# Kernel optimization log

Hardware: AMD Instinct MI355X
Metric: run time of the kernel (lower is better)

Reference implementation:

```python
import jax, jax.numpy as jnp
import numpy as np

B, T, D, H = 128, 512, 1024, 1024


def setup_inputs() -> dict:
    key = jax.random.key(0)
    ks = jax.random.split(key, 9)
    s = 1.0 / np.sqrt(D + H)
    return {
        "inputs": jax.random.normal(ks[0], (B, T, D), dtype=jnp.float32),
        "Wf": jax.random.normal(ks[1], (D + H, H), dtype=jnp.float32) * s,
        "bf": jax.random.normal(ks[2], (H,), dtype=jnp.float32) * s,
        "Wi": jax.random.normal(ks[3], (D + H, H), dtype=jnp.float32) * s,
        "bi": jax.random.normal(ks[4], (H,), dtype=jnp.float32) * s,
        "Wo": jax.random.normal(ks[5], (D + H, H), dtype=jnp.float32) * s,
        "bo": jax.random.normal(ks[6], (H,), dtype=jnp.float32) * s,
        "Wc": jax.random.normal(ks[7], (D + H, H), dtype=jnp.float32) * s,
        "bc": jax.random.normal(ks[8], (H,), dtype=jnp.float32) * s,
    }


def reference(inputs, Wf, bf, Wi, bi, Wo, bo, Wc, bc):
    # inputs: [B, T, D]; gates computed from concat(x_t, h_t) @ W + b.
    # Fuse the 4 gate Linears into one GEMM (same math, single contraction).
    batch = inputs.shape[0]
    hid = Wf.shape[1]
    W = jnp.concatenate([Wf, Wi, Wo, Wc], axis=1)          # [D+H, 4H]
    b = jnp.concatenate([bf, bi, bo, bc])                   # [4H]

    def step(carry, x_t):
        h, c = carry
        z = jnp.concatenate([x_t, h], axis=1) @ W + b        # [B, 4H]
        f, i, o, g = jnp.split(z, 4, axis=1)
        f = jax.nn.sigmoid(f)
        i = jax.nn.sigmoid(i)
        o = jax.nn.sigmoid(o)
        g = jnp.tanh(g)
        c = f * c + i * g
        h = o * jnp.tanh(c)
        return (h, c), h

    h0 = jnp.zeros((batch, hid), dtype=inputs.dtype)
    c0 = jnp.zeros((batch, hid), dtype=inputs.dtype)
    _, hs = jax.lax.scan(step, (h0, c0), jnp.swapaxes(inputs, 0, 1))  # hs: [T, B, H]
    # Original prepends each new hidden state -> outputs are in REVERSE time order.
    return jnp.flip(jnp.swapaxes(hs, 0, 1), axis=1)          # [B, T, H]
```

## Files before the change

### kernel.cpp

```cpp
#include <hip/hip_runtime.h>
#include <hip/hip_bf16.h>

#define Bb 128
#define Tt 512
#define Dd 1024
#define Hh 1024
#define KD 2048
#define CCH 32
#define NCHUNK (Tt / CCH)
#define NBLK 256

typedef __attribute__((ext_vector_type(4))) float f32x4;
typedef __attribute__((ext_vector_type(8))) short s16x8;
typedef __attribute__((address_space(1))) const void gcvoid;
typedef __attribute__((address_space(3))) void lvoid;

__device__ __forceinline__ unsigned short f2bf(float f) {
    union { float f; unsigned u; } v;
    v.f = f;
    unsigned r = v.u + 0x7fffu + ((v.u >> 16) & 1u);
    return (unsigned short)(r >> 16);
}

__device__ __forceinline__ s16x8 cvt8(const float* src) {
    f32x4 a = *reinterpret_cast<const f32x4*>(src);
    f32x4 b = *reinterpret_cast<const f32x4*>(src + 4);
    s16x8 v;
    v[0] = (short)f2bf(a[0]); v[1] = (short)f2bf(a[1]);
    v[2] = (short)f2bf(a[2]); v[3] = (short)f2bf(a[3]);
    v[4] = (short)f2bf(b[0]); v[5] = (short)f2bf(b[1]);
    v[6] = (short)f2bf(b[2]); v[7] = (short)f2bf(b[3]);
    return v;
}

__device__ __forceinline__ float sigf(float x)      { return 1.f / (1.f + __expf(-x)); }
__device__ __forceinline__ float tanhfast(float x)  { return 1.f - 2.f / (1.f + __expf(2.f * x)); }

__device__ __forceinline__ void cstore2(unsigned short* p, unsigned v) {
    asm volatile("global_store_short %0, %1, off sc1" :: "v"(p), "v"(v) : "memory");
}

__device__ __forceinline__ void gbar(unsigned* cntA, unsigned* cntB,
                                     unsigned* flag, int t, int bid) {
    asm volatile("s_waitcnt vmcnt(0)" ::: "memory");
    __syncthreads();
    if (threadIdx.x == 0) {
        unsigned* ca = cntA + ((size_t)t * 8 + (bid & 7)) * 32;
        unsigned o = __hip_atomic_fetch_add(ca, 1u, __ATOMIC_RELAXED, __HIP_MEMORY_SCOPE_AGENT);
        if (o == 31u) {
            unsigned* cb = cntB + (size_t)t * 32;
            unsigned o2 = __hip_atomic_fetch_add(cb, 1u, __ATOMIC_RELAXED, __HIP_MEMORY_SCOPE_AGENT);
            if (o2 == 7u)
                __hip_atomic_store(flag + t, 1u, __ATOMIC_RELAXED, __HIP_MEMORY_SCOPE_AGENT);
        }
        while (__hip_atomic_load(flag + t, __ATOMIC_RELAXED, __HIP_MEMORY_SCOPE_AGENT) == 0u)
            __builtin_amdgcn_s_sleep(1);
    }
    __syncthreads();
}

__global__ __launch_bounds__(256) void zx_gemm(
    const float* __restrict__ X, const unsigned short* __restrict__ Wr,
    const float* __restrict__ bre, float* __restrict__ Zxc, int t0)
{
    __shared__ __align__(16) unsigned short ALds[2][128 * 64];
    __shared__ __align__(16) unsigned short BLds[2][128 * 64];

    const int tid = threadIdx.x, lane = tid & 63, wv = tid >> 6;
    const int wr = wv >> 1, wc = wv & 1;
    const int m0 = (blockIdx.x >> 5) * 128, n0 = (blockIdx.x & 31) * 128;

    f32x4 acc[4][4];
#pragma unroll
    for (int i = 0; i < 4; ++i)
#pragma unroll
        for (int jn = 0; jn < 4; ++jn) acc[i][jn] = 0.f;

    auto stage = [&](int buf, int ki) {
        const int k0 = ki * 64;
#pragma unroll
        for (int i = 0; i < 4; ++i) {
            int slot = i * 256 + tid;
            int r = slot >> 3, cp = slot & 7;
            int c = cp ^ (r & 7);
            int m = m0 + r, b = m >> 5, tc = m & 31;
            const float* src = X + ((size_t)b * Tt + t0 + tc) * Dd + k0 + c * 8;
            *reinterpret_cast<s16x8*>(&ALds[buf][slot * 8]) = cvt8(src);
        }
#pragma unroll
        for (int i = 0; i < 4; ++i) {
            int slot = i * 256 + tid;
            int r = slot >> 3, cp = slot & 7;
            int c = cp ^ (r & 7);
            const unsigned short* src = Wr + (size_t)(n0 + r) * KD + k0 + c * 8;
            __builtin_amdgcn_global_load_lds((gcvoid*)src,
                (lvoid*)&BLds[buf][(i * 256 + wv * 64) * 8], 16, 0, 0);
        }
    };

    auto compute = [&](int buf) {
#pragma unroll
        for (int ks = 0; ks < 2; ++ks) {
            int ck = ks * 4 + (lane >> 4);
            s16x8 af[4], bf8[4];
#pragma unroll
            for (int m = 0; m < 4; ++m) {
                int ra = wr * 64 + m * 16 + (lane & 15);
                af[m] = *reinterpret_cast<const s16x8*>(&ALds[buf][ra * 64 + (ck ^ (ra & 7)) * 8]);
            }
#pragma unroll
            for (int n = 0; n < 4; ++n) {
                int rb = wc * 64 + n * 16 + (lane & 15);
                bf8[n] = *reinterpret_cast<const s16x8*>(&BLds[buf][rb * 64 + (ck ^ (rb & 7)) * 8]);
            }
#pragma unroll
            for (int m = 0; m < 4; ++m)
#pragma unroll
                for (int n = 0; n < 4; ++n)
                    acc[m][n] = __builtin_amdgcn_mfma_f32_16x16x32_bf16(af[m], bf8[n], acc[m][n], 0, 0, 0);
        }
    };

    stage(0, 0);
#pragma unroll 1
    for (int ki = 0; ki < 16; ++ki) {
        __syncthreads();
        if (ki + 1 < 16) stage((ki + 1) & 1, ki + 1);
        compute(ki & 1);
    }

#pragma unroll
    for (int ni = 0; ni < 4; ++ni) {
        int gcol = n0 + wc * 64 + ni * 16 + (lane & 15);
        float bias = bre[gcol];
        int gg = gcol >> 5, nn = gcol & 31;
        int zcol = gg * 32 + (nn & 7) * 4 + (nn >> 3);
#pragma unroll
        for (int mi = 0; mi < 4; ++mi) {
            int rbase = m0 + wr * 64 + mi * 16 + (lane >> 4) * 4;
#pragma unroll
            for (int r = 0; r < 4; ++r)
                Zxc[(size_t)(rbase + r) * 4096 + zcol] = acc[mi][ni][r] + bias;
        }
    }
}

__global__ __launch_bounds__(256) void lstm_chunk(
    const unsigned short* __restrict__ Wr,
    const float* __restrict__ Zxc,
    unsigned short* __restrict__ hring,
    float* __restrict__ cbuf,
    float* __restrict__ out,
    unsigned* __restrict__ cntA,
    unsigned* __restrict__ cntB,
    unsigned* __restrict__ flag,
    int t0)
{
    __shared__ __align__(16) unsigned short Bl[32 * 1024];

    const int tid = threadIdx.x, lane = tid & 63, w = tid >> 6;
    const int bid = blockIdx.x;
    const int g = bid >> 1, mh = bid & 1;

#pragma unroll
    for (int i = 0; i < 16; ++i) {
        int q = (w * 16 + i) * 64 + lane;
        int n = q >> 7, cp = q & 127;
        int cs = (cp & ~7) | ((cp ^ n) & 7);
        const unsigned short* src = Wr + (size_t)(g * 32 + n) * KD + Dd + cs * 8;
        __builtin_amdgcn_global_load_lds((gcvoid*)src,
            (lvoid*)&Bl[(w * 16 + i) * 512], 16, 0, 0);
    }
    asm volatile("s_waitcnt vmcnt(0)" ::: "memory");
    __syncthreads();

    const int nlo = lane & 15;
    const int r0 = mh * 64 + w * 16 + nlo;
    const unsigned short* b0p = &Bl[nlo * 1024];
    const int jj = lane & 7, j = g * 8 + jj;
    const bool hi = (lane & 8) != 0;
    const int rowb = mh * 64 + w * 16 + (lane >> 4) * 4;

    f32x4 creg;
#pragma unroll
    for (int r = 0; r < 4; ++r)
        creg[r] = cbuf[(size_t)(rowb + r) * Hh + j];

    f32x4 zx[4];
#pragma unroll
    for (int r = 0; r < 4; ++r)
        zx[r] = *reinterpret_cast<const f32x4*>(
            Zxc + ((size_t)(rowb + r) * CCH + 0) * 4096 + j * 4);

#pragma unroll 1
    for (int tt = 0; tt < CCH; ++tt) {
        const int t = t0 + tt;
        const unsigned short* hin = hring + (size_t)(t & (CCH - 1)) * (Bb * Hh);
        unsigned short* houtp = hring + (size_t)((t + 1) & (CCH - 1)) * (Bb * Hh);
        const unsigned short* arow = hin + (size_t)r0 * Hh + (lane >> 4) * 8;

        s16x8 af[32];
#pragma unroll
        for (int ki = 0; ki < 32; ++ki)
            af[ki] = *reinterpret_cast<const s16x8*>(arow + ki * 32);

        f32x4 acc0 = 0.f, acc1 = 0.f;
#pragma unroll
        for (int ki = 0; ki < 32; ++ki) {
            int ck = ki * 4 + (lane >> 4);
            int p = (ck & ~7) | ((ck ^ nlo) & 7);
            s16x8 b0 = *reinterpret_cast<const s16x8*>(b0p + p * 8);
            s16x8 b1 = *reinterpret_cast<const s16x8*>(b0p + 16 * 1024 + p * 8);
            acc0 = __builtin_amdgcn_mfma_f32_16x16x32_bf16(af[ki], b0, acc0, 0, 0, 0);
            acc1 = __builtin_amdgcn_mfma_f32_16x16x32_bf16(af[ki], b1, acc1, 0, 0, 0);
        }

        f32x4 y0, y1;
#pragma unroll
        for (int r = 0; r < 4; ++r) {
            y0[r] = __shfl_xor(acc0[r], 8, 64);
            y1[r] = __shfl_xor(acc1[r], 8, 64);
        }

        f32x4 zxn[4];
        if (tt + 1 < CCH) {
#pragma unroll
            for (int r = 0; r < 4; ++r)
                zxn[r] = *reinterpret_cast<const f32x4*>(
                    Zxc + ((size_t)(rowb + r) * CCH + (tt + 1)) * 4096 + j * 4);
        }

#pragma unroll
        for (int r = 0; r < 4; ++r) {
            float vf = hi ? y0[r] : acc0[r];
            float vi = hi ? acc0[r] : y0[r];
            float vo = hi ? y1[r] : acc1[r];
            float vg = hi ? acc1[r] : y1[r];
            float zf = vf + zx[r][0], zi = vi + zx[r][1];
            float zo = vo + zx[r][2], zc = vg + zx[r][3];
            float fg = sigf(zf), ig = sigf(zi), og = sigf(zo), gv = tanhfast(zc);
            float cnew = fg * creg[r] + ig * gv;
            creg[r] = cnew;
            float hn = og * tanhfast(cnew);
            if (!hi) {
                int row = rowb + r;
                cstore2(houtp + (size_t)row * Hh + j, (unsigned)f2bf(hn));
                out[((size_t)row * Tt + (Tt - 1 - t)) * Hh + j] = hn;
            }
        }
#pragma unroll
        for (int r = 0; r < 4; ++r) zx[r] = zxn[r];

        if (tt + 1 < CCH) gbar(cntA, cntB, flag, t, bid);
    }

    if (!hi) {
#pragma unroll
        for (int r = 0; r < 4; ++r)
            cbuf[(size_t)(rowb + r) * Hh + j] = creg[r];
    }
}

__global__ __launch_bounds__(256) void conv_w(
    const float* __restrict__ Wf, const float* __restrict__ Wi,
    const float* __restrict__ Wo, const float* __restrict__ Wc,
    unsigned short* __restrict__ Wr)
{
    __shared__ float sm[64 * 65];
    const int tid = threadIdx.x;
    const int bid = blockIdx.x;
    const int gate = bid & 3;
    const int rest = bid >> 2;
    const int k0 = (rest & 31) * 64;
    const int c0 = (rest >> 5) * 64;
    const float* Wg = (gate == 0) ? Wf : (gate == 1) ? Wi : (gate == 2) ? Wo : Wc;

#pragma unroll
    for (int it = 0; it < 16; ++it) {
        int kl = it * 4 + (tid >> 6), cl = tid & 63;
        sm[kl * 65 + cl] = Wg[(size_t)(k0 + kl) * Hh + c0 + cl];
    }
    __syncthreads();
#pragma unroll
    for (int it = 0; it < 16; ++it) {
        int nl = it * 4 + (tid >> 6), kl = tid & 63;
        int col = c0 + nl;
        int n = (col >> 3) * 32 + gate * 8 + (col & 7);
        Wr[(size_t)n * KD + k0 + kl] = f2bf(sm[kl * 65 + nl]);
    }
}

#define NBAR_U32 (512 * 8 * 32 + 512 * 32 + 512)

__global__ void init_all(unsigned short* __restrict__ hring, float* __restrict__ cbuf,
                         unsigned* __restrict__ bars, float* __restrict__ bre,
                         const float* __restrict__ bF, const float* __restrict__ bI,
                         const float* __restrict__ bO, const float* __restrict__ bC) {
    int i = blockIdx.x * 256 + threadIdx.x;
    if (i < 2 * Bb * Hh) hring[i] = 0;
    if (i < Bb * Hh) cbuf[i] = 0.f;
    if (i < NBAR_U32) bars[i] = 0u;
    if (i < 4096) {
        int gate = (i >> 3) & 3, g = i >> 5, jjv = i & 7;
        int col = g * 8 + jjv;
        const float* bg = (gate == 0) ? bF : (gate == 1) ? bI : (gate == 2) ? bO : bC;
        bre[i] = bg[col];
    }
}

__global__ __launch_bounds__(256) void lstm_step(
    const float* __restrict__ X, const unsigned short* __restrict__ Wr,
    const float* __restrict__ bre,
    const unsigned short* __restrict__ hin, unsigned short* __restrict__ hout,
    float* __restrict__ cbuf, float* __restrict__ out, int t)
{
    __shared__ __align__(16) unsigned short Alds[2][64 * 64];
    __shared__ __align__(16) unsigned short Blds[2][32 * 64];
    __shared__ float zlds[64 * 33];

    const int tid = threadIdx.x, lane = tid & 63, w = tid >> 6;
    const int g = blockIdx.x >> 1, mh = blockIdx.x & 1;

    f32x4 acc[2];
    acc[0] = 0.f; acc[1] = 0.f;

    auto stageA = [&](int buf, int ki) {
        const int k0 = ki * 64;
#pragma unroll
        for (int i = 0; i < 2; ++i) {
            int slot = tid + 256 * i;
            int r = slot >> 3, cp = slot & 7;
            int c = cp ^ (r & 7);
            int k = k0 + c * 8;
            s16x8 v;
            if (k < Dd) {
                v = cvt8(X + ((size_t)(mh * 64 + r) * Tt + t) * Dd + k);
            } else {
                v = *reinterpret_cast<const s16x8*>(hin + (size_t)(mh * 64 + r) * Hh + (k - Dd));
            }
            *reinterpret_cast<s16x8*>(&Alds[buf][slot * 8]) = v;
        }
    };
    auto stageB = [&](int buf, int ki) {
        int n = tid >> 3, cp = tid & 7;
        int c = cp ^ (n & 7);
        const unsigned short* src = Wr + (size_t)(g * 32 + n) * KD + ki * 64 + c * 8;
        *reinterpret_cast<s16x8*>(&Blds[buf][tid * 8]) = *reinterpret_cast<const s16x8*>(src);
    };
    auto compute = [&](int buf) {
#pragma unroll
        for (int ks = 0; ks < 2; ++ks) {
            int ra = w * 16 + (lane & 15);
            int cha = (ks * 4 + (lane >> 4)) ^ (ra & 7);
            s16x8 af = *reinterpret_cast<const s16x8*>(&Alds[buf][ra * 64 + cha * 8]);
#pragma unroll
            for (int nt = 0; nt < 2; ++nt) {
                int n = nt * 16 + (lane & 15);
                int chb = (ks * 4 + (lane >> 4)) ^ (n & 7);
                s16x8 bf8 = *reinterpret_cast<const s16x8*>(&Blds[buf][n * 64 + chb * 8]);
                acc[nt] = __builtin_amdgcn_mfma_f32_16x16x32_bf16(af, bf8, acc[nt], 0, 0, 0);
            }
        }
    };

    stageA(0, 0); stageB(0, 0);
#pragma unroll 1
    for (int ki = 0; ki < 32; ++ki) {
        __syncthreads();
        if (ki + 1 < 32) { stageA((ki + 1) & 1, ki + 1); stageB((ki + 1) & 1, ki + 1); }
        compute(ki & 1);
    }

    {
        int rbase = w * 16 + (lane >> 4) * 4;
#pragma unroll
        for (int nt = 0; nt < 2; ++nt) {
            int col = nt * 16 + (lane & 15);
#pragma unroll
            for (int r = 0; r < 4; ++r)
                zlds[(rbase + r) * 33 + col] = acc[nt][r];
        }
    }
    __syncthreads();

#pragma unroll
    for (int it = 0; it < 2; ++it) {
        int idx = tid + it * 256;
        int row = idx >> 3, jj = idx & 7;
        int jx = g * 8 + jj;
        int grow = mh * 64 + row;
        float zf = zlds[row * 33 + jj]      + bre[g * 32 + jj];
        float zi = zlds[row * 33 + 8 + jj]  + bre[g * 32 + 8 + jj];
        float zo = zlds[row * 33 + 16 + jj] + bre[g * 32 + 16 + jj];
        float zc = zlds[row * 33 + 24 + jj] + bre[g * 32 + 24 + jj];
        float fg = sigf(zf), ig = sigf(zi), og = sigf(zo), gv = tanhfast(zc);
        float cold = cbuf[(size_t)grow * Hh + jx];
        float cnew = fg * cold + ig * gv;
        cbuf[(size_t)grow * Hh + jx] = cnew;
        float hn = og * tanhfast(cnew);
        hout[(size_t)grow * Hh + jx] = f2bf(hn);
        out[((size_t)grow * Tt + (Tt - 1 - t)) * Hh + jx] = hn;
    }
}

extern "C" void kernel_launch(void* const* d_in, const int* in_sizes, int n_in,
                              void* d_out, int out_size, void* d_ws, size_t ws_size,
                              hipStream_t stream) {
    (void)in_sizes; (void)n_in; (void)out_size;
    const float* X  = (const float*)d_in[0];
    const float* Wf = (const float*)d_in[1];
    const float* bF = (const float*)d_in[2];
    const float* Wi = (const float*)d_in[3];
    const float* bI = (const float*)d_in[4];
    const float* Wo = (const float*)d_in[5];
    const float* bO = (const float*)d_in[6];
    const float* Wc = (const float*)d_in[7];
    const float* bC = (const float*)d_in[8];
    float* out = (float*)d_out;

    char* ws = (char*)d_ws;
    size_t off = 0;
    auto carve = [&](size_t sz) { char* p = ws + off; off = (off + sz + 255) & ~(size_t)255; return p; };
    unsigned short* Wr    = (unsigned short*)carve((size_t)4096 * KD * 2);
    float*          bre   = (float*)carve(4096 * 4);
    unsigned short* hring = (unsigned short*)carve((size_t)CCH * Bb * Hh * 2);
    float*          cbuf  = (float*)carve((size_t)Bb * Hh * 4);
    unsigned*       bars  = (unsigned*)carve((size_t)NBAR_U32 * 4);
    float*          Zxc   = (float*)carve((size_t)4096 * 4096 * 4);
    const size_t need = off;

    unsigned* cntA = bars;
    unsigned* cntB = bars + 512 * 8 * 32;
    unsigned* flag = bars + 512 * 8 * 32 + 512 * 32;

    conv_w<<<2048, 256, 0, stream>>>(Wf, Wi, Wo, Wc, Wr);
    init_all<<<1024, 256, 0, stream>>>(hring, cbuf, bars, bre, bF, bI, bO, bC);

    int t_resume = 0;
    if (ws_size >= need) {
        const unsigned short* Wr_c = Wr;
        const float* Zxc_c = Zxc;
        for (int c = 0; c < NCHUNK; ++c) {
            int t0 = c * CCH;
            zx_gemm<<<1024, 256, 0, stream>>>(X, Wr, bre, Zxc, t0);
            void* args[] = {(void*)&Wr_c, (void*)&Zxc_c, (void*)&hring, (void*)&cbuf,
                            (void*)&out, (void*)&cntA, (void*)&cntB, (void*)&flag, (void*)&t0};
            hipError_t rc = hipLaunchCooperativeKernel((void*)lstm_chunk, dim3(NBLK),
                                                       dim3(256), args, 0, stream);
            if (rc != hipSuccess) break;
            t_resume = t0 + CCH;
        }
    }

    for (int t = t_resume; t < Tt; ++t) {
        const unsigned short* hin = hring + (size_t)(t & 1) * Bb * Hh;
        unsigned short*      houtp = hring + (size_t)((t + 1) & 1) * Bb * Hh;
        lstm_step<<<256, 256, 0, stream>>>(X, Wr, bre, hin, houtp, cbuf, out, t);
    }
}
```

Baseline: 5.378 ms.

## Replace grid barrier with sentinel-polled hidden-state ring for dataflow sync

Removes the per-timestep global atomic barrier in the cooperative LSTM chunk kernel. Each slot of a 33-entry hidden-state ring is pre-filled with a 0xFFFF sentinel by a new reset kernel, and consumers poll their loaded h fragments with cache-bypassing loads until no sentinel values remain. Blocks can therefore proceed as soon as the data they need is ready, with no grid-wide rendezvous. The risks are spin traffic on global memory, a legitimate bf16 value equal to the sentinel (0xFFFF is a NaN pattern, so unlikely), and an extra ring-reset kernel launched per chunk.

```diff
diff --git a/kernel.cpp b/kernel.cpp
--- a/kernel.cpp
+++ b/kernel.cpp
@@ -9,9 +9,11 @@
 #define CCH 32
 #define NCHUNK (Tt / CCH)
 #define NBLK 256
+#define RING 33
 
 typedef __attribute__((ext_vector_type(4))) float f32x4;
 typedef __attribute__((ext_vector_type(8))) short s16x8;
+typedef __attribute__((ext_vector_type(4))) unsigned u32x4;
 typedef __attribute__((address_space(1))) const void gcvoid;
 typedef __attribute__((address_space(3))) void lvoid;
 
@@ -40,23 +42,15 @@
     asm volatile("global_store_short %0, %1, off sc1" :: "v"(p), "v"(v) : "memory");
 }
 
-__device__ __forceinline__ void gbar(unsigned* cntA, unsigned* cntB,
-                                     unsigned* flag, int t, int bid) {
-    asm volatile("s_waitcnt vmcnt(0)" ::: "memory");
-    __syncthreads();
-    if (threadIdx.x == 0) {
-        unsigned* ca = cntA + ((size_t)t * 8 + (bid & 7)) * 32;
-        unsigned o = __hip_atomic_fetch_add(ca, 1u, __ATOMIC_RELAXED, __HIP_MEMORY_SCOPE_AGENT);
-        if (o == 31u) {
-            unsigned* cb = cntB + (size_t)t * 32;
-            unsigned o2 = __hip_atomic_fetch_add(cb, 1u, __ATOMIC_RELAXED, __HIP_MEMORY_SCOPE_AGENT);
-            if (o2 == 7u)
-                __hip_atomic_store(flag + t, 1u, __ATOMIC_RELAXED, __HIP_MEMORY_SCOPE_AGENT);
-        }
-        while (__hip_atomic_load(flag + t, __ATOMIC_RELAXED, __HIP_MEMORY_SCOPE_AGENT) == 0u)
-            __builtin_amdgcn_s_sleep(1);
-    }
-    __syncthreads();
+__device__ __forceinline__ bool chunk_bad(const s16x8& v) {
+    u32x4 u = *reinterpret_cast<const u32x4*>(&v);
+    bool bad = false;
+#pragma unroll
+    for (int i = 0; i < 4; ++i) {
+        unsigned x = u[i];
+        bad = bad || (x >= 0xFFFF0000u) || ((x & 0xFFFFu) == 0xFFFFu);
+    }
+    return bad;
 }
 
 __global__ __launch_bounds__(256) void zx_gemm(
@@ -151,9 +145,6 @@
     unsigned short* __restrict__ hring,
     float* __restrict__ cbuf,
     float* __restrict__ out,
-    unsigned* __restrict__ cntA,
-    unsigned* __restrict__ cntB,
-    unsigned* __restrict__ flag,
     int t0)
 {
     __shared__ __align__(16) unsigned short Bl[32 * 1024];
@@ -195,14 +186,35 @@
 #pragma unroll 1
     for (int tt = 0; tt < CCH; ++tt) {
         const int t = t0 + tt;
-        const unsigned short* hin = hring + (size_t)(t & (CCH - 1)) * (Bb * Hh);
-        unsigned short* houtp = hring + (size_t)((t + 1) & (CCH - 1)) * (Bb * Hh);
+        const unsigned short* hin = hring + (size_t)(t % RING) * (Bb * Hh);
+        unsigned short* houtp = hring + (size_t)((t + 1) % RING) * (Bb * Hh);
         const unsigned short* arow = hin + (size_t)r0 * Hh + (lane >> 4) * 8;
 
         s16x8 af[32];
 #pragma unroll
         for (int ki = 0; ki < 32; ++ki)
-            af[ki] = *reinterpret_cast<const s16x8*>(arow + ki * 32);
+            asm volatile("global_load_dwordx4 %0, %1, off sc1"
+                         : "=v"(af[ki]) : "v"(arow + ki * 32) : "memory");
+        asm volatile("s_waitcnt vmcnt(0)" ::: "memory");
+        __builtin_amdgcn_sched_barrier(0);
+
+        unsigned miss = 0xFFFFFFFFu;
+        for (;;) {
+            unsigned still = 0;
+#pragma unroll
+            for (int ki = 0; ki < 32; ++ki)
+                if (miss & (1u << ki))
+                    if (chunk_bad(af[ki])) still |= 1u << ki;
+            if (!__any((int)(still != 0u))) break;
+#pragma unroll
+            for (int ki = 0; ki < 32; ++ki)
+                if (still & (1u << ki))
+                    asm volatile("global_load_dwordx4 %0, %1, off sc1"
+                                 : "=v"(af[ki]) : "v"(arow + ki * 32) : "memory");
+            asm volatile("s_waitcnt vmcnt(0)" ::: "memory");
+            miss = still;
+        }
+        __builtin_amdgcn_sched_barrier(0);
 
         f32x4 acc0 = 0.f, acc1 = 0.f;
 #pragma unroll
@@ -250,14 +262,38 @@
         }
 #pragma unroll
         for (int r = 0; r < 4; ++r) zx[r] = zxn[r];
-
-        if (tt + 1 < CCH) gbar(cntA, cntB, flag, t, bid);
     }
 
     if (!hi) {
 #pragma unroll
         for (int r = 0; r < 4; ++r)
             cbuf[(size_t)(rowb + r) * Hh + j] = creg[r];
+    }
+}
+
+__global__ __launch_bounds__(256) void reset_ring(unsigned short* __restrict__ hring,
+                                                  int keep) {
+    int i = blockIdx.x * 256 + threadIdx.x;
+    int rank = i >> 14;
+    int off = i & 16383;
+    int slot = rank + (rank >= keep ? 1 : 0);
+    u32x4 s;
+    s[0] = s[1] = s[2] = s[3] = 0xFFFFFFFFu;
+    *reinterpret_cast<u32x4*>(hring + (size_t)slot * (Bb * Hh) + off * 8) = s;
+}
+
+__global__ void init_all(unsigned short* __restrict__ hring, float* __restrict__ cbuf,
+                         float* __restrict__ bre,
+                         const float* __restrict__ bF, const float* __restrict__ bI,
+                         const float* __restrict__ bO, const float* __restrict__ bC) {
+    int i = blockIdx.x * 256 + threadIdx.x;
+    if (i < 2 * Bb * Hh) hring[i] = 0;
+    if (i < Bb * Hh) cbuf[i] = 0.f;
+    if (i < 4096) {
+        int gate = (i >> 3) & 3, g = i >> 5, jjv = i & 7;
+        int col = g * 8 + jjv;
+        const float* bg = (gate == 0) ? bF : (gate == 1) ? bI : (gate == 2) ? bO : bC;
+        bre[i] = bg[col];
     }
 }
 
@@ -287,24 +323,6 @@
         int col = c0 + nl;
         int n = (col >> 3) * 32 + gate * 8 + (col & 7);
         Wr[(size_t)n * KD + k0 + kl] = f2bf(sm[kl * 65 + nl]);
-    }
-}
-
-#define NBAR_U32 (512 * 8 * 32 + 512 * 32 + 512)
-
-__global__ void init_all(unsigned short* __restrict__ hring, float* __restrict__ cbuf,
-                         unsigned* __restrict__ bars, float* __restrict__ bre,
-                         const float* __restrict__ bF, const float* __restrict__ bI,
-                         const float* __restrict__ bO, const float* __restrict__ bC) {
-    int i = blockIdx.x * 256 + threadIdx.x;
-    if (i < 2 * Bb * Hh) hring[i] = 0;
-    if (i < Bb * Hh) cbuf[i] = 0.f;
-    if (i < NBAR_U32) bars[i] = 0u;
-    if (i < 4096) {
-        int gate = (i >> 3) & 3, g = i >> 5, jjv = i & 7;
-        int col = g * 8 + jjv;
-        const float* bg = (gate == 0) ? bF : (gate == 1) ? bI : (gate == 2) ? bO : bC;
-        bre[i] = bg[col];
     }
 }
 
@@ -423,18 +441,13 @@
     auto carve = [&](size_t sz) { char* p = ws + off; off = (off + sz + 255) & ~(size_t)255; return p; };
     unsigned short* Wr    = (unsigned short*)carve((size_t)4096 * KD * 2);
     float*          bre   = (float*)carve(4096 * 4);
-    unsigned short* hring = (unsigned short*)carve((size_t)CCH * Bb * Hh * 2);
+    unsigned short* hring = (unsigned short*)carve((size_t)RING * Bb * Hh * 2);
     float*          cbuf  = (float*)carve((size_t)Bb * Hh * 4);
-    unsigned*       bars  = (unsigned*)carve((size_t)NBAR_U32 * 4);
     float*          Zxc   = (float*)carve((size_t)4096 * 4096 * 4);
     const size_t need = off;
 
-    unsigned* cntA = bars;
-    unsigned* cntB = bars + 512 * 8 * 32;
-    unsigned* flag = bars + 512 * 8 * 32 + 512 * 32;
-
     conv_w<<<2048, 256, 0, stream>>>(Wf, Wi, Wo, Wc, Wr);
-    init_all<<<1024, 256, 0, stream>>>(hring, cbuf, bars, bre, bF, bI, bO, bC);
+    init_all<<<1024, 256, 0, stream>>>(hring, cbuf, bre, bF, bI, bO, bC);
 
     int t_resume = 0;
     if (ws_size >= need) {
@@ -442,9 +455,10 @@
         const float* Zxc_c = Zxc;
         for (int c = 0; c < NCHUNK; ++c) {
             int t0 = c * CCH;
+            reset_ring<<<2048, 256, 0, stream>>>(hring, t0 % RING);
             zx_gemm<<<1024, 256, 0, stream>>>(X, Wr, bre, Zxc, t0);
             void* args[] = {(void*)&Wr_c, (void*)&Zxc_c, (void*)&hring, (void*)&cbuf,
-                            (void*)&out, (void*)&cntA, (void*)&cntB, (void*)&flag, (void*)&t0};
+                            (void*)&out, (void*)&t0};
             hipError_t rc = hipLaunchCooperativeKernel((void*)lstm_chunk, dim3(NBLK),
                                                        dim3(256), args, 0, stream);
             if (rc != hipSuccess) break;
@@ -453,8 +467,10 @@
     }
 
     for (int t = t_resume; t < Tt; ++t) {
-        const unsigned short* hin = hring + (size_t)(t & 1) * Bb * Hh;
-        unsigned short*      houtp = hring + (size_t)((t + 1) & 1) * Bb * Hh;
+        const unsigned short* hin = (t == t_resume)
+            ? hring + (size_t)(t_resume % RING) * (Bb * Hh)
+            : hring + (size_t)(t & 1) * (Bb * Hh);
+        unsigned short* houtp = hring + (size_t)((t + 1) & 1) * (Bb * Hh);
         lstm_step<<<256, 256, 0, stream>>>(X, Wr, bre, hin, houtp, cbuf, out, t);
     }
 }
```

After: 9.938 ms. +84.8%, slower.

## Overlap next chunk's input GEMM with recurrent LSTM chunk in one cooperative launch

Applied to the files above, without the earlier changes.

Adds 256 extra blocks to the cooperative lstm_chunk launch. These blocks compute the input projection (Zx) for the next time chunk into a second double-buffered Zxc workspace while the recurrent blocks process the current chunk. This removes the serial zx_gemm launch between chunks and hides the GEMM behind the latency-bound recurrence. In exchange it doubles workspace use, and the extra blocks compete with the recurrent blocks for CUs and memory bandwidth, which could slow the spin-barrier steps. Cooperative launch with 512 blocks also needs enough co-residency, otherwise the code falls back to per-step kernels.

```diff
diff --git a/kernel.cpp b/kernel.cpp
--- a/kernel.cpp
+++ b/kernel.cpp
@@ -9,6 +9,7 @@
 #define CCH 32
 #define NCHUNK (Tt / CCH)
 #define NBLK 256
+#define NZXB 256
 
 typedef __attribute__((ext_vector_type(4))) float f32x4;
 typedef __attribute__((ext_vector_type(8))) short s16x8;
@@ -59,16 +60,16 @@
     __syncthreads();
 }
 
-__global__ __launch_bounds__(256) void zx_gemm(
+__device__ __forceinline__ void zx_tile(
     const float* __restrict__ X, const unsigned short* __restrict__ Wr,
-    const float* __restrict__ bre, float* __restrict__ Zxc, int t0)
+    const float* __restrict__ bre, float* __restrict__ Zxc,
+    int t0, int m0, int n0, unsigned char* smem)
 {
-    __shared__ __align__(16) unsigned short ALds[2][128 * 64];
-    __shared__ __align__(16) unsigned short BLds[2][128 * 64];
+    unsigned short* ALds = (unsigned short*)smem;
+    unsigned short* BLds = (unsigned short*)(smem + 32768);
 
     const int tid = threadIdx.x, lane = tid & 63, wv = tid >> 6;
     const int wr = wv >> 1, wc = wv & 1;
-    const int m0 = (blockIdx.x >> 5) * 128, n0 = (blockIdx.x & 31) * 128;
 
     f32x4 acc[4][4];
 #pragma unroll
@@ -85,7 +86,7 @@
             int c = cp ^ (r & 7);
             int m = m0 + r, b = m >> 5, tc = m & 31;
             const float* src = X + ((size_t)b * Tt + t0 + tc) * Dd + k0 + c * 8;
-            *reinterpret_cast<s16x8*>(&ALds[buf][slot * 8]) = cvt8(src);
+            *reinterpret_cast<s16x8*>(&ALds[buf * 8192 + slot * 8]) = cvt8(src);
         }
 #pragma unroll
         for (int i = 0; i < 4; ++i) {
@@ -94,7 +95,7 @@
             int c = cp ^ (r & 7);
             const unsigned short* src = Wr + (size_t)(n0 + r) * KD + k0 + c * 8;
             __builtin_amdgcn_global_load_lds((gcvoid*)src,
-                (lvoid*)&BLds[buf][(i * 256 + wv * 64) * 8], 16, 0, 0);
+                (lvoid*)&BLds[buf * 8192 + (i * 256 + wv * 64) * 8], 16, 0, 0);
         }
     };
 
@@ -106,12 +107,12 @@
 #pragma unroll
             for (int m = 0; m < 4; ++m) {
                 int ra = wr * 64 + m * 16 + (lane & 15);
-                af[m] = *reinterpret_cast<const s16x8*>(&ALds[buf][ra * 64 + (ck ^ (ra & 7)) * 8]);
+                af[m] = *reinterpret_cast<const s16x8*>(&ALds[buf * 8192 + ra * 64 + (ck ^ (ra & 7)) * 8]);
             }
 #pragma unroll
             for (int n = 0; n < 4; ++n) {
                 int rb = wc * 64 + n * 16 + (lane & 15);
-                bf8[n] = *reinterpret_cast<const s16x8*>(&BLds[buf][rb * 64 + (ck ^ (rb & 7)) * 8]);
+                bf8[n] = *reinterpret_cast<const s16x8*>(&BLds[buf * 8192 + rb * 64 + (ck ^ (rb & 7)) * 8]);
             }
 #pragma unroll
             for (int m = 0; m < 4; ++m)
@@ -145,21 +146,50 @@
     }
 }
 
+__global__ __launch_bounds__(256) void zx_gemm(
+    const float* __restrict__ X, const unsigned short* __restrict__ Wr,
+    const float* __restrict__ bre, float* __restrict__ Zxc, int t0)
+{
+    __shared__ __align__(16) unsigned char smem[65536];
+    const int tile = blockIdx.x;
+    zx_tile(X, Wr, bre, Zxc, t0, (tile >> 5) * 128, (tile & 31) * 128, smem);
+}
+
 __global__ __launch_bounds__(256) void lstm_chunk(
+    const float* __restrict__ X,
     const unsigned short* __restrict__ Wr,
-    const float* __restrict__ Zxc,
+    const float* __restrict__ ZxcRead,
+    float* __restrict__ ZxcWrite,
+    const float* __restrict__ bre,
     unsigned short* __restrict__ hring,
     float* __restrict__ cbuf,
     float* __restrict__ out,
     unsigned* __restrict__ cntA,
     unsigned* __restrict__ cntB,
     unsigned* __restrict__ flag,
-    int t0)
+    int t0, int t0z)
 {
-    __shared__ __align__(16) unsigned short Bl[32 * 1024];
+    __shared__ __align__(16) unsigned char smem[65536];
+
+    const int bid = blockIdx.x;
+
+    if (bid >= NBLK) {
+        if (t0z < Tt) {
+            const int zbid = bid - NBLK;
+#pragma unroll 1
+            for (int q = 0; q < 4; ++q) {
+                int tile = zbid + NZXB * q;
+                zx_tile(X, Wr, bre, ZxcWrite, t0z,
+                        (tile >> 5) * 128, (tile & 31) * 128, smem);
+                __syncthreads();
+            }
+        }
+        return;
+    }
+
+    unsigned short* Bl = (unsigned short*)smem;
 
     const int tid = threadIdx.x, lane = tid & 63, w = tid >> 6;
-    const int bid = blockIdx.x;
     const int g = bid >> 1, mh = bid & 1;
 
 #pragma unroll
@@ -190,7 +220,7 @@
 #pragma unroll
     for (int r = 0; r < 4; ++r)
         zx[r] = *reinterpret_cast<const f32x4*>(
-            Zxc + ((size_t)(rowb + r) * CCH + 0) * 4096 + j * 4);
+            ZxcRead + ((size_t)(rowb + r) * CCH + 0) * 4096 + j * 4);
 
 #pragma unroll 1
     for (int tt = 0; tt < CCH; ++tt) {
@@ -227,7 +257,7 @@
 #pragma unroll
             for (int r = 0; r < 4; ++r)
                 zxn[r] = *reinterpret_cast<const f32x4*>(
-                    Zxc + ((size_t)(rowb + r) * CCH + (tt + 1)) * 4096 + j * 4);
+                    ZxcRead + ((size_t)(rowb + r) * CCH + (tt + 1)) * 4096 + j * 4);
         }
 
 #pragma unroll
@@ -426,8 +456,10 @@
     unsigned short* hring = (unsigned short*)carve((size_t)CCH * Bb * Hh * 2);
     float*          cbuf  = (float*)carve((size_t)Bb * Hh * 4);
     unsigned*       bars  = (unsigned*)carve((size_t)NBAR_U32 * 4);
-    float*          Zxc   = (float*)carve((size_t)4096 * 4096 * 4);
-    const size_t need = off;
+    float*          Zxc0  = (float*)carve((size_t)4096 * 4096 * 4);
+    const size_t need_r12 = off;
+    float*          Zxc1  = (float*)carve((size_t)4096 * 4096 * 4);
+    const size_t need_big = off;
 
     unsigned* cntA = bars;
     unsigned* cntB = bars + 512 * 8 * 32;
@@ -436,17 +468,41 @@
     conv_w<<<2048, 256, 0, stream>>>(Wf, Wi, Wo, Wc, Wr);
     init_all<<<1024, 256, 0, stream>>>(hring, cbuf, bars, bre, bF, bI, bO, bC);
 
+    const bool fused = (ws_size >= need_big);
+    const bool r12ok = (ws_size >= need_r12);
+
     int t_resume = 0;
-    if (ws_size >= need) {
-        const unsigned short* Wr_c = Wr;
-        const float* Zxc_c = Zxc;
+    if (fused) {
+        zx_gemm<<<1024, 256, 0, stream>>>(X, Wr, bre, Zxc0, 0);
         for (int c = 0; c < NCHUNK; ++c) {
             int t0 = c * CCH;
-            zx_gemm<<<1024, 256, 0, stream>>>(X, Wr, bre, Zxc, t0);
-            void* args[] = {(void*)&Wr_c, (void*)&Zxc_c, (void*)&hring, (void*)&cbuf,
-                            (void*)&out, (void*)&cntA, (void*)&cntB, (void*)&flag, (void*)&t0};
-            hipError_t rc = hipLaunchCooperativeKernel((void*)lstm_chunk, dim3(NBLK),
-                                                       dim3(256), args, 0, stream);
+            int t0z = t0 + CCH;
+            const float* zrd = (c & 1) ? Zxc1 : Zxc0;
+            float*       zwr = (c & 1) ? Zxc0 : Zxc1;
+            void* args[] = {(void*)&X, (void*)&Wr, (void*)&zrd, (void*)&zwr, (void*)&bre,
+                            (void*)&hring, (void*)&cbuf, (void*)&out,
+                            (void*)&cntA, (void*)&cntB, (void*)&flag,
+                            (void*)&t0, (void*)&t0z};
+            hipError_t rc = hipLaunchCooperativeKernel((void*)lstm_chunk,
+                                                       dim3(NBLK + NZXB), dim3(256),
+                                                       args, 0, stream);
+            if (rc != hipSuccess) break;
+            t_resume = t0 + CCH;
+        }
+    } else if (r12ok) {
+        for (int c = 0; c < NCHUNK; ++c) {
+            int t0 = c * CCH;
+            int t0z = Tt;
+            const float* zrd = Zxc0;
+            float*       zwr = Zxc0;
+            zx_gemm<<<1024, 256, 0, stream>>>(X, Wr, bre, Zxc0, t0);
+            void* args[] = {(void*)&X, (void*)&Wr, (void*)&zrd, (void*)&zwr, (void*)&bre,
+                            (void*)&hring, (void*)&cbuf, (void*)&out,
+                            (void*)&cntA, (void*)&cntB, (void*)&flag,
+                            (void*)&t0, (void*)&t0z};
+            hipError_t rc = hipLaunchCooperativeKernel((void*)lstm_chunk,
+                                                       dim3(NBLK), dim3(256),
+                                                       args, 0, stream);
             if (rc != hipSuccess) break;
             t_resume = t0 + CCH;
         }
```

Result: slower. 21.39 ms (+297.8%).
